# Optimization experiments

Measured on AMD Instinct MI355X. Metric: run time of the kernel, lower is better.

The kernel has to match this reference:

```python
import jax, jax.numpy as jnp
import numpy as np

EMBED_DIM = 1024
NUM_HEADS = 16
HEAD_DIM = EMBED_DIM // NUM_HEADS
B, L = 2, 2048


def setup_inputs() -> dict:
    key = jax.random.key(0)
    k1, k2, k3, k4, k5, k6 = jax.random.split(key, 6)
    x = jax.random.normal(k1, (B, L, EMBED_DIM), dtype=jnp.float32)
    freqs_cis = jax.random.normal(k2, (L, HEAD_DIM // 2, 2), dtype=jnp.float32)
    attn_bias = jax.random.normal(k3, (1, NUM_HEADS, L, L), dtype=jnp.float32)
    s = 1.0 / np.sqrt(EMBED_DIM)
    w_qkv = jax.random.normal(k4, (EMBED_DIM, 3 * EMBED_DIM), dtype=jnp.float32) * s
    w_proj = jax.random.normal(k5, (EMBED_DIM, EMBED_DIM), dtype=jnp.float32) * s
    b_proj = jax.random.normal(k6, (EMBED_DIM,), dtype=jnp.float32) * 0.01
    return {"x": x, "freqs_cis": freqs_cis, "attn_bias": attn_bias,
            "w_qkv": w_qkv, "w_proj": w_proj, "b_proj": b_proj}


def _apply_rope(t, freqs):
    # t: [B, L, H, hd]; freqs: [L, hd//2, 2]
    Bq, Lq, H, hd = t.shape
    t2 = t.reshape(Bq, Lq, H, hd // 2, 2)
    fc = freqs[None, :, None, :, :]  # [1, L, 1, hd//2, 2]
    real = t2[..., 0] * fc[..., 0] - t2[..., 1] * fc[..., 1]
    imag = t2[..., 1] * fc[..., 0] + t2[..., 0] * fc[..., 1]
    return jnp.stack([real, imag], axis=-1).reshape(Bq, Lq, H, hd)


def reference(x, freqs_cis, attn_bias, w_qkv, w_proj, b_proj):
    Bq, Lq, C = x.shape
    qkv = x @ w_qkv  # [B, L, 3C]
    q, k, v = jnp.split(qkv, 3, axis=-1)
    q = q.reshape(Bq, Lq, NUM_HEADS, HEAD_DIM)
    k = k.reshape(Bq, Lq, NUM_HEADS, HEAD_DIM)
    v = v.reshape(Bq, Lq, NUM_HEADS, HEAD_DIM)
    q = _apply_rope(q, freqs_cis)
    k = _apply_rope(k, freqs_cis)
    scale = HEAD_DIM ** -0.5
    # scores: [B, H, L, L]
    scores = jnp.einsum('bqhd,bkhd->bhqk', q, k) * scale + attn_bias
    weights = jax.nn.softmax(scores, axis=-1)
    out = jnp.einsum('bhqk,bkhd->bqhd', weights, v).reshape(Bq, Lq, C)
    return out @ w_proj + b_proj
```

## Files before the change

kernel.cpp:

```cpp
#include <hip/hip_runtime.h>
#include <hip/hip_bf16.h>
#include <cstddef>

#define L_SEQ 2048
#define CDIM  1024
#define NH    16
#define HD    64

typedef __attribute__((ext_vector_type(8))) short bf16x8;
typedef __attribute__((ext_vector_type(4))) float f32x4;

typedef __attribute__((address_space(3))) unsigned int lds_uint;
typedef const __attribute__((address_space(1))) unsigned int glob_uint;

__device__ __forceinline__ void gll16(const void* g, void* l) {
    __builtin_amdgcn_global_load_lds((glob_uint*)g, (lds_uint*)l, 16, 0, 0);
}
__device__ __forceinline__ short f2bf(float f) {
    __hip_bfloat16 h = __float2bfloat16(f);
    return *reinterpret_cast<short*>(&h);
}
__device__ __forceinline__ float bf2f(short s) {
    __hip_bfloat16 h = *reinterpret_cast<__hip_bfloat16*>(&s);
    return __bfloat162float(h);
}

__global__ __launch_bounds__(256) void cast_bf16(
    const float* __restrict__ src, short* __restrict__ dst, int n8)
{
    int t = blockIdx.x * 256 + threadIdx.x;
    if (t >= n8) return;
    float4 a = ((const float4*)src)[t * 2];
    float4 b = ((const float4*)src)[t * 2 + 1];
    short tmp[8] = { f2bf(a.x), f2bf(a.y), f2bf(a.z), f2bf(a.w),
                     f2bf(b.x), f2bf(b.y), f2bf(b.z), f2bf(b.w) };
    ((uint4*)dst)[t] = *(uint4*)tmp;
}

__global__ __launch_bounds__(256) void transpose_cast(
    const float* __restrict__ W, short* __restrict__ WT, int K, int N)
{
    __shared__ float t[64][65];
    const int n0 = blockIdx.x * 64, k0 = blockIdx.y * 64;
    const int tid = threadIdx.x;
#pragma unroll
    for (int j = 0; j < 4; ++j) {
        int e = tid + j * 256;
        int r = e >> 4, c4 = e & 15;
        *(float4*)&t[r][c4 * 4] = *(const float4*)(W + (size_t)(k0 + r) * N + n0 + c4 * 4);
    }
    __syncthreads();
#pragma unroll
    for (int j = 0; j < 2; ++j) {
        int e = tid + j * 256;
        int nr = e >> 3, c8 = (e & 7) * 8;
        short tmp[8];
#pragma unroll
        for (int i = 0; i < 8; ++i) tmp[i] = f2bf(t[c8 + i][nr]);
        *(uint4*)(WT + (size_t)(n0 + nr) * K + k0 + c8) = *(uint4*)tmp;
    }
}

__global__ __launch_bounds__(256) void gemm_qkv(
    const short* __restrict__ A, const short* __restrict__ BT,
    short* __restrict__ Qb, short* __restrict__ Kb, short* __restrict__ Vt)
{
    __shared__ short As[128 * 32];
    __shared__ short Bs[128 * 32];
    const int tid = threadIdx.x;
    const int w = tid >> 6, lane = tid & 63;
    const int m0 = blockIdx.y * 128, n0 = blockIdx.x * 128;
    const int K = CDIM;
    const int rsub = lane >> 2;
    const int kcol = (lane & 3) * 8;
    f32x4 acc[4][4] = {};

    for (int k0 = 0; k0 < K; k0 += 32) {
#pragma unroll
        for (int seg = 0; seg < 2; ++seg) {
            int r = w * 32 + seg * 16 + rsub;
            gll16(A  + (size_t)(m0 + r) * K + k0 + kcol, &As[(w * 32 + seg * 16) * 32]);
            gll16(BT + (size_t)(n0 + r) * K + k0 + kcol, &Bs[(w * 32 + seg * 16) * 32]);
        }
        __syncthreads();
        bf16x8 af[4], bfr[4];
#pragma unroll
        for (int i = 0; i < 4; ++i) {
            af[i]  = *(const bf16x8*)&As[((w >> 1) * 64 + i * 16 + (lane & 15)) * 32 + (lane >> 4) * 8];
            bfr[i] = *(const bf16x8*)&Bs[((w & 1)  * 64 + i * 16 + (lane & 15)) * 32 + (lane >> 4) * 8];
        }
#pragma unroll
        for (int i = 0; i < 4; ++i)
#pragma unroll
            for (int j = 0; j < 4; ++j)
                acc[i][j] = __builtin_amdgcn_mfma_f32_16x16x32_bf16(af[i], bfr[j], acc[i][j], 0, 0, 0);
        __syncthreads();
    }

    const int region = n0 >> 10;
    const int wr = w >> 1, wc = w & 1;
    const int crow = (lane >> 4) * 4, ccol = lane & 15;
#pragma unroll
    for (int i = 0; i < 4; ++i)
#pragma unroll
        for (int j = 0; j < 4; ++j) {
            int n = n0 + wc * 64 + j * 16 + ccol;
            int cc = n & 1023, h = cc >> 6, d = cc & 63;
#pragma unroll
            for (int r = 0; r < 4; ++r) {
                int m = m0 + wr * 64 + i * 16 + crow + r;
                int bb = m >> 11, l = m & (L_SEQ - 1);
                short v = f2bf(acc[i][j][r]);
                if (region == 0)
                    Qb[(size_t)((bb * NH + h) * L_SEQ + l) * HD + d] = v;
                else if (region == 1)
                    Kb[(size_t)((bb * NH + h) * L_SEQ + l) * HD + d] = v;
                else
                    Vt[(size_t)((bb * NH + h) * HD + d) * L_SEQ + l] = v;
            }
        }
}

__global__ __launch_bounds__(256) void rope_kernel(
    short* __restrict__ Qb, short* __restrict__ Kb, const float* __restrict__ freqs)
{
    int t = blockIdx.x * 256 + threadIdx.x;
    short* P = blockIdx.y ? Kb : Qb;
    const float qs = blockIdx.y ? 1.0f : 0.125f;
    const int d0 = (t * 8) & (HD - 1);
    const int l  = (t >> 3) & (L_SEQ - 1);
    uint4 raw = ((uint4*)P)[t];
    short* s = (short*)&raw;
    const float* fr = freqs + l * HD + d0;
    float f[8];
    *(float4*)&f[0] = *(const float4*)fr;
    *(float4*)&f[4] = *(const float4*)(fr + 4);
    short outv[8];
#pragma unroll
    for (int p = 0; p < 4; ++p) {
        float a = bf2f(s[2 * p]), b = bf2f(s[2 * p + 1]);
        outv[2 * p]     = f2bf((a * f[2 * p] - b * f[2 * p + 1]) * qs);
        outv[2 * p + 1] = f2bf((b * f[2 * p] + a * f[2 * p + 1]) * qs);
    }
    ((uint4*)P)[t] = *(uint4*)outv;
}

__global__ __launch_bounds__(256) void attn_mfma(
    const short* __restrict__ Qb, const short* __restrict__ Kb,
    const short* __restrict__ Vt, const float* __restrict__ bias,
    short* __restrict__ Ab)
{
    __shared__ short Qs[64][72];
    __shared__ short Ks[64][72];
    __shared__ short Vs[64][72];
    __shared__ short Ps[4][16][72];
    const int tid = threadIdx.x, w = tid >> 6, lane = tid & 63;
    const int q0 = blockIdx.x * 64, h = blockIdx.y, b = blockIdx.z;
    const short* Qp = Qb + (size_t)((b * NH + h) * L_SEQ + q0) * HD;
    const short* Kp = Kb + (size_t)((b * NH + h) * L_SEQ) * HD;
    const short* Vp = Vt + (size_t)((b * NH + h) * HD) * L_SEQ;
    const float* bp = bias + (size_t)h * L_SEQ * L_SEQ + (size_t)q0 * L_SEQ;

#pragma unroll
    for (int j = 0; j < 2; ++j) {
        int e = tid + j * 256;
        int r = e >> 3, c8 = (e & 7) * 8;
        *(uint4*)&Qs[r][c8] = *(const uint4*)(Qp + (size_t)r * HD + c8);
    }

    const int g = lane >> 4, c = lane & 15;
    float m_run[4], l_run[4];
    f32x4 oacc[4] = {};
#pragma unroll
    for (int r = 0; r < 4; ++r) { m_run[r] = -1e30f; l_run[r] = 0.f; }

    for (int kt = 0; kt < L_SEQ / 64; ++kt) {
        const int k0 = kt * 64;
        __syncthreads();
#pragma unroll
        for (int j = 0; j < 2; ++j) {
            int e = tid + j * 256;
            int r = e >> 3, c8 = (e & 7) * 8;
            *(uint4*)&Ks[r][c8] = *(const uint4*)(Kp + (size_t)(k0 + r) * HD + c8);
            *(uint4*)&Vs[r][c8] = *(const uint4*)(Vp + (size_t)r * L_SEQ + k0 + c8);
        }
        f32x4 sacc[4];
#pragma unroll
        for (int j = 0; j < 4; ++j)
#pragma unroll
            for (int r = 0; r < 4; ++r)
                sacc[j][r] = bp[(size_t)(w * 16 + g * 4 + r) * L_SEQ + k0 + j * 16 + c];
        __syncthreads();

#pragma unroll
        for (int kb = 0; kb < 2; ++kb) {
            bf16x8 aq = *(const bf16x8*)&Qs[w * 16 + c][kb * 32 + g * 8];
#pragma unroll
            for (int j = 0; j < 4; ++j) {
                bf16x8 bk = *(const bf16x8*)&Ks[j * 16 + c][kb * 32 + g * 8];
                sacc[j] = __builtin_amdgcn_mfma_f32_16x16x32_bf16(aq, bk, sacc[j], 0, 0, 0);
            }
        }

        float mnew[4], pv[4][4];
#pragma unroll
        for (int r = 0; r < 4; ++r) {
            float tmv = fmaxf(fmaxf(sacc[0][r], sacc[1][r]), fmaxf(sacc[2][r], sacc[3][r]));
#pragma unroll
            for (int off = 1; off < 16; off <<= 1)
                tmv = fmaxf(tmv, __shfl_xor(tmv, off, 64));
            mnew[r] = fmaxf(m_run[r], tmv);
        }
#pragma unroll
        for (int r = 0; r < 4; ++r) {
            float acc = 0.f;
#pragma unroll
            for (int j = 0; j < 4; ++j) { pv[j][r] = __expf(sacc[j][r] - mnew[r]); acc += pv[j][r]; }
#pragma unroll
            for (int off = 1; off < 16; off <<= 1) acc += __shfl_xor(acc, off, 64);
            float fct = __expf(m_run[r] - mnew[r]);
            l_run[r] = l_run[r] * fct + acc;
            m_run[r] = mnew[r];
#pragma unroll
            for (int di = 0; di < 4; ++di) oacc[di][r] *= fct;
        }

#pragma unroll
        for (int j = 0; j < 4; ++j)
#pragma unroll
            for (int r = 0; r < 4; ++r)
                Ps[w][g * 4 + r][j * 16 + c] = f2bf(pv[j][r]);
        asm volatile("" ::: "memory");

#pragma unroll
        for (int kb = 0; kb < 2; ++kb) {
            bf16x8 pa = *(const bf16x8*)&Ps[w][c][kb * 32 + g * 8];
#pragma unroll
            for (int di = 0; di < 4; ++di) {
                bf16x8 vb = *(const bf16x8*)&Vs[di * 16 + c][kb * 32 + g * 8];
                oacc[di] = __builtin_amdgcn_mfma_f32_16x16x32_bf16(pa, vb, oacc[di], 0, 0, 0);
            }
        }
    }

#pragma unroll
    for (int di = 0; di < 4; ++di)
#pragma unroll
        for (int r = 0; r < 4; ++r) {
            int m = b * L_SEQ + q0 + w * 16 + g * 4 + r;
            int col = h * HD + di * 16 + c;
            Ab[(size_t)m * CDIM + col] = f2bf(oacc[di][r] / l_run[r]);
        }
}

__global__ __launch_bounds__(256) void gemm_proj(
    const short* __restrict__ A, const short* __restrict__ BT,
    const float* __restrict__ bprj, float* __restrict__ out)
{
    __shared__ short As[128 * 32];
    __shared__ short Bs[128 * 32];
    const int tid = threadIdx.x;
    const int w = tid >> 6, lane = tid & 63;
    const int m0 = blockIdx.y * 128, n0 = blockIdx.x * 128;
    const int K = CDIM;
    const int rsub = lane >> 2;
    const int kcol = (lane & 3) * 8;
    f32x4 acc[4][4] = {};

    for (int k0 = 0; k0 < K; k0 += 32) {
#pragma unroll
        for (int seg = 0; seg < 2; ++seg) {
            int r = w * 32 + seg * 16 + rsub;
            gll16(A  + (size_t)(m0 + r) * K + k0 + kcol, &As[(w * 32 + seg * 16) * 32]);
            gll16(BT + (size_t)(n0 + r) * K + k0 + kcol, &Bs[(w * 32 + seg * 16) * 32]);
        }
        __syncthreads();
        bf16x8 af[4], bfr[4];
#pragma unroll
        for (int i = 0; i < 4; ++i) {
            af[i]  = *(const bf16x8*)&As[((w >> 1) * 64 + i * 16 + (lane & 15)) * 32 + (lane >> 4) * 8];
            bfr[i] = *(const bf16x8*)&Bs[((w & 1)  * 64 + i * 16 + (lane & 15)) * 32 + (lane >> 4) * 8];
        }
#pragma unroll
        for (int i = 0; i < 4; ++i)
#pragma unroll
            for (int j = 0; j < 4; ++j)
                acc[i][j] = __builtin_amdgcn_mfma_f32_16x16x32_bf16(af[i], bfr[j], acc[i][j], 0, 0, 0);
        __syncthreads();
    }

    const int wr = w >> 1, wc = w & 1;
    const int crow = (lane >> 4) * 4, ccol = lane & 15;
#pragma unroll
    for (int i = 0; i < 4; ++i)
#pragma unroll
        for (int j = 0; j < 4; ++j) {
            int n = n0 + wc * 64 + j * 16 + ccol;
            float bv = bprj[n];
#pragma unroll
            for (int r = 0; r < 4; ++r) {
                int m = m0 + wr * 64 + i * 16 + crow + r;
                out[(size_t)m * CDIM + n] = acc[i][j][r] + bv;
            }
        }
}

extern "C" void kernel_launch(void* const* d_in, const int* in_sizes, int n_in,
                              void* d_out, int out_size, void* d_ws, size_t ws_size,
                              hipStream_t stream) {
    const float* x     = (const float*)d_in[0];
    const float* freqs = (const float*)d_in[1];
    const float* bias  = (const float*)d_in[2];
    const float* w_qkv = (const float*)d_in[3];
    const float* w_prj = (const float*)d_in[4];
    const float* b_prj = (const float*)d_in[5];
    float* out = (float*)d_out;

    short* ws = (short*)d_ws;
    short* xb     = ws;
    short* wqkvT  = xb + 4194304;
    short* wprojT = wqkvT + 3145728;
    short* Qb     = wprojT + 1048576;
    short* Kb     = Qb + 4194304;
    short* Vt     = Kb + 4194304;
    short* Ab     = Vt + 4194304;

    cast_bf16<<<2048, 256, 0, stream>>>(x, xb, 524288);
    transpose_cast<<<dim3(48, 16), 256, 0, stream>>>(w_qkv, wqkvT, CDIM, 3 * CDIM);
    transpose_cast<<<dim3(16, 16), 256, 0, stream>>>(w_prj, wprojT, CDIM, CDIM);
    gemm_qkv<<<dim3(24, 32), 256, 0, stream>>>(xb, wqkvT, Qb, Kb, Vt);
    rope_kernel<<<dim3(2048, 2), 256, 0, stream>>>(Qb, Kb, freqs);
    attn_mfma<<<dim3(32, NH, 2), 256, 0, stream>>>(Qb, Kb, Vt, bias, Ab);
    gemm_proj<<<dim3(8, 32), 256, 0, stream>>>(Ab, wprojT, b_prj, out);
}
```

Measured before the change: 534.3 us.

## Fuse RoPE into QKV GEMM, prefetch attention tiles, shrink projection tile

RoPE and the query scaling move into the QKV GEMM epilogue, which uses lane shuffles to fetch the paired element, so the separate rope kernel and its extra read and write of Q/K are gone. The attention kernel keeps Q in registers, prefetches the next K/V tiles and bias into registers to overlap global loads with compute, and rescales the running output only when some row's max grows. The projection GEMM uses 128x64 tiles so it launches twice as many blocks for better occupancy. The changes add register pressure in attention and some scattered freqs loads in the GEMM epilogue.

```diff
diff --git a/kernel.cpp b/kernel.cpp
--- a/kernel.cpp
+++ b/kernel.cpp
@@ -63,6 +63,7 @@
 
 __global__ __launch_bounds__(256) void gemm_qkv(
     const short* __restrict__ A, const short* __restrict__ BT,
+    const float* __restrict__ freqs,
     short* __restrict__ Qb, short* __restrict__ Kb, short* __restrict__ Vt)
 {
     __shared__ short As[128 * 32];
@@ -100,49 +101,43 @@
     const int region = n0 >> 10;
     const int wr = w >> 1, wc = w & 1;
     const int crow = (lane >> 4) * 4, ccol = lane & 15;
-#pragma unroll
-    for (int i = 0; i < 4; ++i)
-#pragma unroll
-        for (int j = 0; j < 4; ++j) {
-            int n = n0 + wc * 64 + j * 16 + ccol;
-            int cc = n & 1023, h = cc >> 6, d = cc & 63;
+
+    if (region == 2) {
+#pragma unroll
+        for (int i = 0; i < 4; ++i)
+#pragma unroll
+            for (int j = 0; j < 4; ++j) {
+                int cc = (n0 & 1023) + wc * 64 + j * 16 + ccol;
+                int h = cc >> 6, d = cc & 63;
+#pragma unroll
+                for (int r = 0; r < 4; ++r) {
+                    int m = m0 + wr * 64 + i * 16 + crow + r;
+                    int bb = m >> 11, l = m & (L_SEQ - 1);
+                    Vt[((size_t)(bb * NH + h) * HD + d) * L_SEQ + l] = f2bf(acc[i][j][r]);
+                }
+            }
+    } else {
+        const float qs = (region == 0) ? 0.125f : 1.0f;
+        short* dst = (region == 0) ? Qb : Kb;
+#pragma unroll
+        for (int i = 0; i < 4; ++i)
 #pragma unroll
             for (int r = 0; r < 4; ++r) {
                 int m = m0 + wr * 64 + i * 16 + crow + r;
                 int bb = m >> 11, l = m & (L_SEQ - 1);
-                short v = f2bf(acc[i][j][r]);
-                if (region == 0)
-                    Qb[(size_t)((bb * NH + h) * L_SEQ + l) * HD + d] = v;
-                else if (region == 1)
-                    Kb[(size_t)((bb * NH + h) * L_SEQ + l) * HD + d] = v;
-                else
-                    Vt[(size_t)((bb * NH + h) * HD + d) * L_SEQ + l] = v;
-            }
-        }
-}
-
-__global__ __launch_bounds__(256) void rope_kernel(
-    short* __restrict__ Qb, short* __restrict__ Kb, const float* __restrict__ freqs)
-{
-    int t = blockIdx.x * 256 + threadIdx.x;
-    short* P = blockIdx.y ? Kb : Qb;
-    const float qs = blockIdx.y ? 1.0f : 0.125f;
-    const int d0 = (t * 8) & (HD - 1);
-    const int l  = (t >> 3) & (L_SEQ - 1);
-    uint4 raw = ((uint4*)P)[t];
-    short* s = (short*)&raw;
-    const float* fr = freqs + l * HD + d0;
-    float f[8];
-    *(float4*)&f[0] = *(const float4*)fr;
-    *(float4*)&f[4] = *(const float4*)(fr + 4);
-    short outv[8];
-#pragma unroll
-    for (int p = 0; p < 4; ++p) {
-        float a = bf2f(s[2 * p]), b = bf2f(s[2 * p + 1]);
-        outv[2 * p]     = f2bf((a * f[2 * p] - b * f[2 * p + 1]) * qs);
-        outv[2 * p + 1] = f2bf((b * f[2 * p] + a * f[2 * p + 1]) * qs);
-    }
-    ((uint4*)P)[t] = *(uint4*)outv;
+#pragma unroll
+                for (int j = 0; j < 4; ++j) {
+                    int cc = (n0 & 1023) + wc * 64 + j * 16 + ccol;
+                    int h = cc >> 6, d = cc & 63;
+                    float v  = acc[i][j][r];
+                    float vp = __shfl_xor(v, 1, 64);
+                    float fo = freqs[l * HD + d];
+                    float fp = __shfl_xor(fo, 1, 64);
+                    float o = (d & 1) ? (v * fp + vp * fo) : (v * fo - vp * fp);
+                    dst[((size_t)(bb * NH + h) * L_SEQ + l) * HD + d] = f2bf(o * qs);
+                }
+            }
+    }
 }
 
 __global__ __launch_bounds__(256) void attn_mfma(
@@ -150,86 +145,114 @@
     const short* __restrict__ Vt, const float* __restrict__ bias,
     short* __restrict__ Ab)
 {
-    __shared__ short Qs[64][72];
     __shared__ short Ks[64][72];
     __shared__ short Vs[64][72];
     __shared__ short Ps[4][16][72];
     const int tid = threadIdx.x, w = tid >> 6, lane = tid & 63;
     const int q0 = blockIdx.x * 64, h = blockIdx.y, b = blockIdx.z;
+    const int g = lane >> 4, c = lane & 15;
     const short* Qp = Qb + (size_t)((b * NH + h) * L_SEQ + q0) * HD;
     const short* Kp = Kb + (size_t)((b * NH + h) * L_SEQ) * HD;
     const short* Vp = Vt + (size_t)((b * NH + h) * HD) * L_SEQ;
     const float* bp = bias + (size_t)h * L_SEQ * L_SEQ + (size_t)q0 * L_SEQ;
 
-#pragma unroll
-    for (int j = 0; j < 2; ++j) {
-        int e = tid + j * 256;
-        int r = e >> 3, c8 = (e & 7) * 8;
-        *(uint4*)&Qs[r][c8] = *(const uint4*)(Qp + (size_t)r * HD + c8);
-    }
-
-    const int g = lane >> 4, c = lane & 15;
+    bf16x8 aq0 = *(const bf16x8*)(Qp + (w * 16 + c) * HD + g * 8);
+    bf16x8 aq1 = *(const bf16x8*)(Qp + (w * 16 + c) * HD + 32 + g * 8);
+
+    const int srow = tid >> 3;
+    const int scol = (tid & 7) * 8;
+
     float m_run[4], l_run[4];
     f32x4 oacc[4] = {};
 #pragma unroll
     for (int r = 0; r < 4; ++r) { m_run[r] = -1e30f; l_run[r] = 0.f; }
 
+    uint4 kr0 = *(const uint4*)(Kp + (size_t)srow * HD + scol);
+    uint4 kr1 = *(const uint4*)(Kp + (size_t)(srow + 32) * HD + scol);
+    uint4 vr0 = *(const uint4*)(Vp + (size_t)srow * L_SEQ + scol);
+    uint4 vr1 = *(const uint4*)(Vp + (size_t)(srow + 32) * L_SEQ + scol);
+    float br[4][4];
+#pragma unroll
+    for (int j = 0; j < 4; ++j)
+#pragma unroll
+        for (int r = 0; r < 4; ++r)
+            br[j][r] = bp[(size_t)(w * 16 + g * 4 + r) * L_SEQ + j * 16 + c];
+
     for (int kt = 0; kt < L_SEQ / 64; ++kt) {
-        const int k0 = kt * 64;
-        __syncthreads();
-#pragma unroll
-        for (int j = 0; j < 2; ++j) {
-            int e = tid + j * 256;
-            int r = e >> 3, c8 = (e & 7) * 8;
-            *(uint4*)&Ks[r][c8] = *(const uint4*)(Kp + (size_t)(k0 + r) * HD + c8);
-            *(uint4*)&Vs[r][c8] = *(const uint4*)(Vp + (size_t)r * L_SEQ + k0 + c8);
-        }
+        __syncthreads();
+        *(uint4*)&Ks[srow][scol]      = kr0;
+        *(uint4*)&Ks[srow + 32][scol] = kr1;
+        *(uint4*)&Vs[srow][scol]      = vr0;
+        *(uint4*)&Vs[srow + 32][scol] = vr1;
         f32x4 sacc[4];
 #pragma unroll
         for (int j = 0; j < 4; ++j)
 #pragma unroll
-            for (int r = 0; r < 4; ++r)
-                sacc[j][r] = bp[(size_t)(w * 16 + g * 4 + r) * L_SEQ + k0 + j * 16 + c];
-        __syncthreads();
-
-#pragma unroll
-        for (int kb = 0; kb < 2; ++kb) {
-            bf16x8 aq = *(const bf16x8*)&Qs[w * 16 + c][kb * 32 + g * 8];
-#pragma unroll
-            for (int j = 0; j < 4; ++j) {
-                bf16x8 bk = *(const bf16x8*)&Ks[j * 16 + c][kb * 32 + g * 8];
-                sacc[j] = __builtin_amdgcn_mfma_f32_16x16x32_bf16(aq, bk, sacc[j], 0, 0, 0);
-            }
-        }
-
-        float mnew[4], pv[4][4];
+            for (int r = 0; r < 4; ++r) sacc[j][r] = br[j][r];
+        __syncthreads();
+
+        if (kt + 1 < L_SEQ / 64) {
+            const int kn = (kt + 1) * 64;
+            kr0 = *(const uint4*)(Kp + (size_t)(kn + srow) * HD + scol);
+            kr1 = *(const uint4*)(Kp + (size_t)(kn + srow + 32) * HD + scol);
+            vr0 = *(const uint4*)(Vp + (size_t)srow * L_SEQ + kn + scol);
+            vr1 = *(const uint4*)(Vp + (size_t)(srow + 32) * L_SEQ + kn + scol);
+#pragma unroll
+            for (int j = 0; j < 4; ++j)
+#pragma unroll
+                for (int r = 0; r < 4; ++r)
+                    br[j][r] = bp[(size_t)(w * 16 + g * 4 + r) * L_SEQ + kn + j * 16 + c];
+        }
+
+#pragma unroll
+        for (int j = 0; j < 4; ++j) {
+            bf16x8 bk0 = *(const bf16x8*)&Ks[j * 16 + c][g * 8];
+            sacc[j] = __builtin_amdgcn_mfma_f32_16x16x32_bf16(aq0, bk0, sacc[j], 0, 0, 0);
+            bf16x8 bk1 = *(const bf16x8*)&Ks[j * 16 + c][32 + g * 8];
+            sacc[j] = __builtin_amdgcn_mfma_f32_16x16x32_bf16(aq1, bk1, sacc[j], 0, 0, 0);
+        }
+
+        float tmv[4];
 #pragma unroll
         for (int r = 0; r < 4; ++r) {
-            float tmv = fmaxf(fmaxf(sacc[0][r], sacc[1][r]), fmaxf(sacc[2][r], sacc[3][r]));
+            float t0 = fmaxf(fmaxf(sacc[0][r], sacc[1][r]), fmaxf(sacc[2][r], sacc[3][r]));
 #pragma unroll
             for (int off = 1; off < 16; off <<= 1)
-                tmv = fmaxf(tmv, __shfl_xor(tmv, off, 64));
-            mnew[r] = fmaxf(m_run[r], tmv);
+                t0 = fmaxf(t0, __shfl_xor(t0, off, 64));
+            tmv[r] = t0;
+        }
+        int grow = 0;
+#pragma unroll
+        for (int r = 0; r < 4; ++r) grow |= (tmv[r] > m_run[r]) ? 1 : 0;
+        if (__any(grow)) {
+#pragma unroll
+            for (int r = 0; r < 4; ++r) {
+                float mn = fmaxf(m_run[r], tmv[r]);
+                float fct = __expf(m_run[r] - mn);
+                l_run[r] *= fct;
+                m_run[r] = mn;
+#pragma unroll
+                for (int di = 0; di < 4; ++di) oacc[di][r] *= fct;
+            }
         }
 #pragma unroll
         for (int r = 0; r < 4; ++r) {
             float acc = 0.f;
 #pragma unroll
-            for (int j = 0; j < 4; ++j) { pv[j][r] = __expf(sacc[j][r] - mnew[r]); acc += pv[j][r]; }
+            for (int j = 0; j < 4; ++j) {
+                sacc[j][r] = __expf(sacc[j][r] - m_run[r]);
+                acc += sacc[j][r];
+            }
 #pragma unroll
             for (int off = 1; off < 16; off <<= 1) acc += __shfl_xor(acc, off, 64);
-            float fct = __expf(m_run[r] - mnew[r]);
-            l_run[r] = l_run[r] * fct + acc;
-            m_run[r] = mnew[r];
-#pragma unroll
-            for (int di = 0; di < 4; ++di) oacc[di][r] *= fct;
+            l_run[r] += acc;
         }
 
 #pragma unroll
         for (int j = 0; j < 4; ++j)
 #pragma unroll
             for (int r = 0; r < 4; ++r)
-                Ps[w][g * 4 + r][j * 16 + c] = f2bf(pv[j][r]);
+                Ps[w][g * 4 + r][j * 16 + c] = f2bf(sacc[j][r]);
         asm volatile("" ::: "memory");
 
 #pragma unroll
@@ -258,33 +281,37 @@
     const float* __restrict__ bprj, float* __restrict__ out)
 {
     __shared__ short As[128 * 32];
-    __shared__ short Bs[128 * 32];
+    __shared__ short Bs[64 * 32];
     const int tid = threadIdx.x;
     const int w = tid >> 6, lane = tid & 63;
-    const int m0 = blockIdx.y * 128, n0 = blockIdx.x * 128;
+    const int m0 = blockIdx.y * 128, n0 = blockIdx.x * 64;
     const int K = CDIM;
     const int rsub = lane >> 2;
     const int kcol = (lane & 3) * 8;
-    f32x4 acc[4][4] = {};
+    f32x4 acc[4][2] = {};
 
     for (int k0 = 0; k0 < K; k0 += 32) {
 #pragma unroll
         for (int seg = 0; seg < 2; ++seg) {
             int r = w * 32 + seg * 16 + rsub;
-            gll16(A  + (size_t)(m0 + r) * K + k0 + kcol, &As[(w * 32 + seg * 16) * 32]);
-            gll16(BT + (size_t)(n0 + r) * K + k0 + kcol, &Bs[(w * 32 + seg * 16) * 32]);
-        }
-        __syncthreads();
-        bf16x8 af[4], bfr[4];
-#pragma unroll
-        for (int i = 0; i < 4; ++i) {
-            af[i]  = *(const bf16x8*)&As[((w >> 1) * 64 + i * 16 + (lane & 15)) * 32 + (lane >> 4) * 8];
-            bfr[i] = *(const bf16x8*)&Bs[((w & 1)  * 64 + i * 16 + (lane & 15)) * 32 + (lane >> 4) * 8];
-        }
-#pragma unroll
-        for (int i = 0; i < 4; ++i)
-#pragma unroll
-            for (int j = 0; j < 4; ++j)
+            gll16(A + (size_t)(m0 + r) * K + k0 + kcol, &As[(w * 32 + seg * 16) * 32]);
+        }
+        {
+            int r = w * 16 + rsub;
+            gll16(BT + (size_t)(n0 + r) * K + k0 + kcol, &Bs[(w * 16) * 32]);
+        }
+        __syncthreads();
+        bf16x8 af[4], bfr[2];
+#pragma unroll
+        for (int i = 0; i < 4; ++i)
+            af[i] = *(const bf16x8*)&As[((w >> 1) * 64 + i * 16 + (lane & 15)) * 32 + (lane >> 4) * 8];
+#pragma unroll
+        for (int j = 0; j < 2; ++j)
+            bfr[j] = *(const bf16x8*)&Bs[((w & 1) * 32 + j * 16 + (lane & 15)) * 32 + (lane >> 4) * 8];
+#pragma unroll
+        for (int i = 0; i < 4; ++i)
+#pragma unroll
+            for (int j = 0; j < 2; ++j)
                 acc[i][j] = __builtin_amdgcn_mfma_f32_16x16x32_bf16(af[i], bfr[j], acc[i][j], 0, 0, 0);
         __syncthreads();
     }
@@ -294,8 +321,8 @@
 #pragma unroll
     for (int i = 0; i < 4; ++i)
 #pragma unroll
-        for (int j = 0; j < 4; ++j) {
-            int n = n0 + wc * 64 + j * 16 + ccol;
+        for (int j = 0; j < 2; ++j) {
+            int n = n0 + wc * 32 + j * 16 + ccol;
             float bv = bprj[n];
 #pragma unroll
             for (int r = 0; r < 4; ++r) {
@@ -328,8 +355,7 @@
     cast_bf16<<<2048, 256, 0, stream>>>(x, xb, 524288);
     transpose_cast<<<dim3(48, 16), 256, 0, stream>>>(w_qkv, wqkvT, CDIM, 3 * CDIM);
     transpose_cast<<<dim3(16, 16), 256, 0, stream>>>(w_prj, wprojT, CDIM, CDIM);
-    gemm_qkv<<<dim3(24, 32), 256, 0, stream>>>(xb, wqkvT, Qb, Kb, Vt);
-    rope_kernel<<<dim3(2048, 2), 256, 0, stream>>>(Qb, Kb, freqs);
+    gemm_qkv<<<dim3(24, 32), 256, 0, stream>>>(xb, wqkvT, freqs, Qb, Kb, Vt);
     attn_mfma<<<dim3(32, NH, 2), 256, 0, stream>>>(Qb, Kb, Vt, bias, Ab);
-    gemm_proj<<<dim3(8, 32), 256, 0, stream>>>(Ab, wprojT, b_prj, out);
-}
+    gemm_proj<<<dim3(16, 32), 256, 0, stream>>>(Ab, wprojT, b_prj, out);
+}
```

Result: slower. 550.2 us (+3.0%).
